# Optimization experiments

Hardware: AMD Instinct MI355X
Metric: run time of the kernel (lower is better)

## Reference

```python
import jax, jax.numpy as jnp
import numpy as np

D_MODEL = 1024
N_HEADS = 16
FEA = 512
BATCH = 16
D_FF = 2048
HALF = D_MODEL // 2  # d_model / 2**fd_num with fd_num=1
INV_SQRT2 = 1.0 / np.sqrt(2.0).astype(np.float32)


def conv1d_circ(x, w, b):
    # x: (B, C_in, L); w: (C_out, C_in, 3); circular padding of 1 each side
    xp = jnp.pad(x, ((0, 0), (0, 0), (1, 1)), mode='wrap')
    y = jax.lax.conv_general_dilated(xp, w, (1,), 'VALID',
                                     dimension_numbers=('NCH', 'OIH', 'NCH'))
    return y + b[None, :, None]


def layer_norm(x, g, b):
    m = jnp.mean(x, axis=-1, keepdims=True)
    v = jnp.mean((x - m) ** 2, axis=-1, keepdims=True)
    return (x - m) / jnp.sqrt(v + 1e-5) * g + b


def setup_inputs() -> dict:
    key = jax.random.key(0)
    ks = jax.random.split(key, 16)
    s = 0.02
    inp = {
        'x': jax.random.normal(ks[0], (BATCH, FEA, D_MODEL), dtype=jnp.float32),
        'Wq': jax.random.normal(ks[1], (D_MODEL, HALF, 3), dtype=jnp.float32) * s,
        'bq': jnp.zeros((D_MODEL,), jnp.float32),
        'Wk': jax.random.normal(ks[2], (D_MODEL, HALF, 3), dtype=jnp.float32) * s,
        'bk': jnp.zeros((D_MODEL,), jnp.float32),
        'Wv': jax.random.normal(ks[3], (D_MODEL, HALF, 3), dtype=jnp.float32) * s,
        'bv': jnp.zeros((D_MODEL,), jnp.float32),
        'uns_w': jax.random.normal(ks[4], (FEA, 2 * FEA, 3), dtype=jnp.float32) * s,
        'uns_b': jnp.zeros((FEA,), jnp.float32),
        'cv_w1': jax.random.normal(ks[5], (D_FF, D_MODEL, 3), dtype=jnp.float32) * s,
        'cv_b1': jnp.zeros((D_FF,), jnp.float32),
        'cv_w2': jax.random.normal(ks[6], (HALF, D_FF, 3), dtype=jnp.float32) * s,
        'cv_b2': jnp.zeros((HALF,), jnp.float32),
        'cv_g': jnp.ones((HALF,), jnp.float32),
        'cv_beta': jnp.zeros((HALF,), jnp.float32),
        'up_w1': jax.random.normal(ks[7], (D_FF, HALF, 3), dtype=jnp.float32) * s,
        'up_b1': jnp.zeros((D_FF,), jnp.float32),
        'up_w2': jax.random.normal(ks[8], (D_MODEL, D_FF, 3), dtype=jnp.float32) * s,
        'up_b2': jnp.zeros((D_MODEL,), jnp.float32),
        'up_g': jnp.ones((D_MODEL,), jnp.float32),
        'up_beta': jnp.zeros((D_MODEL,), jnp.float32),
    }
    return inp


def reference(x, Wq, bq, Wk, bk, Wv, bv, uns_w, uns_b,
              cv_w1, cv_b1, cv_w2, cv_b2, cv_g, cv_beta,
              up_w1, up_b1, up_w2, up_b2, up_g, up_beta):
    x_input = x
    # torch code detaches x before the wavelet transform -> no grad through this branch
    xd = jax.lax.stop_gradient(x)
    # Haar (db1) single-level DWT along last axis (even length -> exact pairwise)
    x1 = (xd[..., 0::2] + xd[..., 1::2]) * INV_SQRT2  # cA: (B, F, HALF)
    x2 = (xd[..., 0::2] - xd[..., 1::2]) * INV_SQRT2  # cD: (B, F, HALF)

    def proj(z, w, b):  # (B, F, HALF) -> (B, F, D_MODEL)
        return conv1d_circ(z.swapaxes(1, 2), w, b).swapaxes(1, 2)

    def heads(z):  # (B, F, D_MODEL) -> (B, H, F, dh)
        b_, f_, _ = z.shape
        return z.reshape(b_, f_, N_HEADS, -1).transpose(0, 2, 1, 3)

    qh, kh, vh = heads(proj(x1, Wq, bq)), heads(proj(x1, Wk, bk)), heads(proj(x1, Wv, bv))
    ql, kl, vl = heads(proj(x2, Wq, bq)), heads(proj(x2, Wk, bk)), heads(proj(x2, Wv, bv))

    scale = 1.0 / np.sqrt(N_HEADS).astype(np.float32)  # note: module scales by sqrt(n_heads)
    b_, f_ = x.shape[0], x.shape[1]

    hp = jax.nn.softmax(jnp.einsum('bhqd,bhkd->bhqk', qh, kl) * scale, axis=-1)
    h_ctx = jnp.einsum('bhqk,bhkd->bhqd', hp, vh).transpose(0, 2, 1, 3).reshape(b_, f_, -1)
    lp = jax.nn.softmax(jnp.einsum('bhqd,bhkd->bhqk', ql, kh) * scale, axis=-1)
    l_ctx = jnp.einsum('bhqk,bhkd->bhqd', lp, vl).transpose(0, 2, 1, 3).reshape(b_, f_, -1)

    ctx = jnp.concatenate([h_ctx, l_ctx], axis=1)          # (B, 2F, D_MODEL)
    ctx = conv1d_circ(ctx, uns_w, uns_b)                    # channels=2F -> F, length=D_MODEL

    # Convlayer: conv over fea axis, channels D_MODEL -> D_FF -> HALF, then LN
    h = conv1d_circ(ctx.swapaxes(1, 2), cv_w1, cv_b1)
    h = conv1d_circ(jax.nn.relu(h), cv_w2, cv_b2)
    ctx = layer_norm(h.swapaxes(1, 2), cv_g, cv_beta)       # (B, F, HALF)

    # upsizeConvlayer: HALF -> D_FF -> D_MODEL, then LN
    h = conv1d_circ(ctx.swapaxes(1, 2), up_w1, up_b1)
    h = conv1d_circ(jax.nn.relu(h), up_w2, up_b2)
    out = layer_norm(h.swapaxes(1, 2), up_g, up_beta)       # (B, F, D_MODEL)
    return out + x_input
```

## Files before the change

kernel.cpp:

```cpp
#include <hip/hip_runtime.h>
#include <hip/hip_bf16.h>

#define B_    16
#define FEA_  512
#define DM_   1024
#define HALF_ 512
#define DFF_  2048

typedef unsigned short u16;
typedef __attribute__((ext_vector_type(8))) short bf16x8;
typedef __attribute__((ext_vector_type(4))) float f32x4;

__device__ __forceinline__ float bf2f(u16 u) {
  union { unsigned int i; float f; } v; v.i = ((unsigned int)u) << 16; return v.f;
}
__device__ __forceinline__ u16 f2bf(float f) {
  union { float f; unsigned int i; } v; v.f = f;
  unsigned int x = v.i;
  return (u16)((x + 0x7fffu + ((x >> 16) & 1u)) >> 16);
}
__device__ __forceinline__ void gload16(const u16* g, u16* l) {
  __builtin_amdgcn_global_load_lds(
      (const __attribute__((address_space(1))) void*)g,
      (__attribute__((address_space(3))) void*)l, 16, 0, 0);
}

__global__ void dwt_kernel(const float* __restrict__ x, u16* __restrict__ x1,
                           u16* __restrict__ x2, int n) {
  int i = blockIdx.x * 256 + threadIdx.x;
  if (i >= n) return;
  float2 v = ((const float2*)x)[i];
  x1[i] = f2bf((v.x + v.y) * 0.70710678118f);
  x2[i] = f2bf((v.x - v.y) * 0.70710678118f);
}

__global__ void wtrans3_kernel(const float* __restrict__ w0, const float* __restrict__ w1,
                               const float* __restrict__ w2, u16* __restrict__ wt,
                               int Cout, int Cin) {
  int n = Cout * Cin * 3;
  int e = blockIdx.x * 256 + threadIdx.x;
  if (e >= 3 * n) return;
  int i = e / n, le = e - i * n;
  const float* w = (i == 0) ? w0 : ((i == 1) ? w1 : w2);
  int co = le / (Cin * 3);
  int r  = le - co * Cin * 3;
  int ci = r / 3;
  int t  = r - ci * 3;
  wt[(size_t)i * n + ((size_t)t * Cout + co) * Cin + ci] = f2bf(w[le]);
}

struct WTSeg { const float* src; u16* dst; int cout, cin, base; };
struct WT5 { WTSeg s[5]; int total; };
__global__ void wtrans5_kernel(WT5 p) {
  int e = blockIdx.x * 256 + threadIdx.x;
  if (e >= p.total) return;
#pragma unroll
  for (int i = 0; i < 5; ++i) {
    int Cin = p.s[i].cin, Cout = p.s[i].cout;
    int n = Cout * Cin * 3;
    int le = e - p.s[i].base;
    if (le >= 0 && le < n) {
      int co = le / (Cin * 3);
      int r  = le - co * Cin * 3;
      int ci = r / 3;
      int t  = r - ci * 3;
      p.s[i].dst[((size_t)t * Cout + co) * Cin + ci] = f2bf(p.s[i].src[le]);
    }
  }
}

#define ZS_GLOAD(c0_)                                                        \
  {                                                                          \
    _Pragma("unroll") for (int i_ = 0; i_ < 5; ++i_) {                       \
      int e_ = tid + i_ * 256;                                               \
      if (e_ < 130 * 8) {                                                    \
        int r_ = e_ >> 3, c_ = e_ & 7;                                       \
        int gl_ = l0 + r_ - 1;                                               \
        if (gl_ < 0) gl_ += L; else if (gl_ >= L) gl_ -= L;                  \
        gload16(Zb + (size_t)gl_ * Cin + (c0_) + ((c_ ^ (r_ & 7)) * 8),      \
                smem + ((size_t)(i_ * 256 + (tid & 192)) * 8));              \
      }                                                                      \
    }                                                                        \
  }
#define WS_ISSUE(t_, c0_, buf_)                                              \
  {                                                                          \
    const u16* Wg_ = Wt + ((size_t)(t_) * Cout + co0) * Cin + (c0_);         \
    int c_ = lane & 7;                                                       \
    _Pragma("unroll") for (int i_ = 0; i_ < 4; ++i_) {                       \
      int rw_ = (i_ * 4 + w) * 8 + (lane >> 3);                              \
      gload16(Wg_ + (size_t)rw_ * Cin + ((c_ ^ (rw_ & 7)) * 8),              \
              &Wb[(buf_)][(i_ * 4 + w) * 8][0]);                             \
    }                                                                        \
  }
#define COMPUTE(t_, buf_)                                                    \
  {                                                                          \
    _Pragma("unroll") for (int ks = 0; ks < 2; ++ks) {                       \
      int s = ks * 4 + g4;                                                   \
      bf16x8 af[4], bfr[4];                                                  \
      _Pragma("unroll") for (int mi = 0; mi < 4; ++mi) {                     \
        int ra = wr * 64 + mi * 16 + row16 + (t_);                           \
        af[mi] = *(const bf16x8*)&Zs[ra][(s ^ (ra & 7)) * 8];                \
      }                                                                      \
      _Pragma("unroll") for (int ni = 0; ni < 4; ++ni) {                     \
        int rb = wc * 64 + ni * 16 + row16;                                  \
        bfr[ni] = *(const bf16x8*)&Wb[(buf_)][rb][(s ^ (rb & 7)) * 8];       \
      }                                                                      \
      __builtin_amdgcn_s_setprio(1);                                         \
      _Pragma("unroll") for (int mi = 0; mi < 4; ++mi)                       \
        _Pragma("unroll") for (int ni = 0; ni < 4; ++ni)                     \
          acc[mi][ni] = __builtin_amdgcn_mfma_f32_16x16x32_bf16(             \
              af[mi], bfr[ni], acc[mi][ni], 0, 0, 0);                        \
      __builtin_amdgcn_s_setprio(0);                                         \
    }                                                                        \
  }
#define COMPUTE2_REG(buf_)                                                   \
  {                                                                          \
    _Pragma("unroll") for (int ks = 0; ks < 2; ++ks) {                       \
      int s = ks * 4 + g4;                                                   \
      bf16x8 bfr[4];                                                         \
      _Pragma("unroll") for (int ni = 0; ni < 4; ++ni) {                     \
        int rb = wc * 64 + ni * 16 + row16;                                  \
        bfr[ni] = *(const bf16x8*)&Wb[(buf_)][rb][(s ^ (rb & 7)) * 8];       \
      }                                                                      \
      __builtin_amdgcn_s_setprio(1);                                         \
      _Pragma("unroll") for (int mi = 0; mi < 4; ++mi)                       \
        _Pragma("unroll") for (int ni = 0; ni < 4; ++ni)                     \
          acc[mi][ni] = __builtin_amdgcn_mfma_f32_16x16x32_bf16(             \
              af2[ks * 4 + mi], bfr[ni], acc[mi][ni], 0, 0, 0);              \
      __builtin_amdgcn_s_setprio(0);                                         \
    }                                                                        \
  }
#define WAIT4 { asm volatile("s_waitcnt vmcnt(4)" ::: "memory");             \
                __builtin_amdgcn_s_barrier(); }

__global__ __launch_bounds__(256, 2) void conv_mfma_kernel(
    const u16* __restrict__ Z, const u16* __restrict__ Wt,
    const float* __restrict__ bias, u16* __restrict__ out,
    int L, int Cin, int Cout, int osl, int osc, int relu) {
  __shared__ __align__(16) u16 smem[130 * 64 + 3 * 128 * 64];
  u16 (*Zs)[64] = (u16(*)[64])smem;
  u16 (*Wb)[128][64] = (u16(*)[128][64])(smem + 130 * 64);
  int l0 = blockIdx.x * 128, co0 = blockIdx.y * 128, b = blockIdx.z;
  int tid = threadIdx.x;
  int lane = tid & 63, w = tid >> 6, wr = w >> 1, wc = w & 1;
  int row16 = lane & 15, g4 = lane >> 4;
  f32x4 acc[4][4];
#pragma unroll
  for (int i = 0; i < 4; ++i)
#pragma unroll
    for (int j = 0; j < 4; ++j) acc[i][j] = (f32x4){0.f, 0.f, 0.f, 0.f};
  const u16* Zb = Z + (size_t)b * L * Cin;

  int ncg = Cin >> 6;
  ZS_GLOAD(0);
  WS_ISSUE(0, 0, 0);
  WS_ISSUE(1, 0, 1);

  for (int cg = 0; cg < ncg; ++cg) {
    int c0 = cg << 6;
    bool lastg = (cg == ncg - 1);
    WAIT4;
    WS_ISSUE(2, c0, 2);
    COMPUTE(0, 0);
    WAIT4;
    if (!lastg) WS_ISSUE(0, c0 + 64, 0);
    COMPUTE(1, 1);
    if (!lastg) {
      WAIT4;
      bf16x8 af2[8];
#pragma unroll
      for (int ks = 0; ks < 2; ++ks) {
        int s = ks * 4 + g4;
#pragma unroll
        for (int mi = 0; mi < 4; ++mi) {
          int ra = wr * 64 + mi * 16 + row16 + 2;
          af2[ks * 4 + mi] = *(const bf16x8*)&Zs[ra][(s ^ (ra & 7)) * 8];
        }
      }
      __builtin_amdgcn_sched_barrier(0);
      asm volatile("s_waitcnt lgkmcnt(0)" ::: "memory");
      __builtin_amdgcn_s_barrier();
      ZS_GLOAD(c0 + 64);
      WS_ISSUE(1, c0 + 64, 1);
      COMPUTE2_REG(2);
    } else {
      asm volatile("s_waitcnt vmcnt(0)" ::: "memory");
      __builtin_amdgcn_s_barrier();
      COMPUTE(2, 2);
    }
  }

  __syncthreads();
  const int TP = 136;
  u16* tile = smem;
  size_t ob = (size_t)b * L * Cout;
  int S, rowbase, colbase;
  if (osc == 1) { S = osl; rowbase = l0; colbase = co0; }
  else          { S = osc; rowbase = co0; colbase = l0; }
#pragma unroll
  for (int ni = 0; ni < 4; ++ni) {
    int c_loc = wc * 64 + ni * 16 + row16;
    float bz = bias[co0 + c_loc];
#pragma unroll
    for (int mi = 0; mi < 4; ++mi) {
#pragma unroll
      for (int r = 0; r < 4; ++r) {
        int l_loc = wr * 64 + mi * 16 + g4 * 4 + r;
        float v = acc[mi][ni][r] + bz;
        if (relu) v = fmaxf(v, 0.f);
        int row = (osc == 1) ? l_loc : c_loc;
        int col = (osc == 1) ? c_loc : l_loc;
        tile[row * TP + col] = f2bf(v);
      }
    }
  }
  __syncthreads();
  for (int e = tid; e < 128 * 16; e += 256) {
    int row = e >> 4, c8 = (e & 15) * 8;
    *(uint4*)(out + ob + (size_t)(rowbase + row) * S + colbase + c8) =
        *(const uint4*)&tile[row * TP + c8];
  }
}

#define AQOFF 0
#define AKOFF 8192
#define AVOFF 20480
#define APOFF 32768
#define AT_Q_STAGE()                                                         \
  { _Pragma("unroll") for (int i_ = 0; i_ < 4; ++i_) {                       \
      int idx_ = tid + i_ * 256; int r_ = idx_ >> 3, c_ = idx_ & 7;          \
      gload16(Qg + (size_t)(q0 + r_) * DM_ + ((c_ ^ (r_ & 7)) * 8),          \
              asm_ + AQOFF + (i_ * 256 + (tid & 192)) * 8); } }
#define AT_K_STAGE(kt_, buf_)                                                \
  { _Pragma("unroll") for (int i_ = 0; i_ < 2; ++i_) {                       \
      int idx_ = tid + i_ * 256; int r_ = idx_ >> 3, c_ = idx_ & 7;          \
      gload16(Kg + (size_t)((kt_) * 64 + r_) * DM_ + ((c_ ^ (r_ & 7)) * 8),  \
              asm_ + AKOFF + (buf_) * 4096 + (i_ * 256 + (tid & 192)) * 8); } }
#define AT_V_STAGE(kt_, buf_)                                                \
  { _Pragma("unroll") for (int i_ = 0; i_ < 2; ++i_) {                       \
      int idx_ = tid + i_ * 256; int r_ = idx_ >> 3, c_ = idx_ & 7;          \
      gload16(Vg + (size_t)r_ * FEA_ + (kt_) * 64 + ((c_ ^ (r_ & 7)) * 8),   \
              asm_ + AVOFF + (buf_) * 4096 + (i_ * 256 + (tid & 192)) * 8); } }
#define LGKM0_BAR { asm volatile("s_waitcnt lgkmcnt(0)" ::: "memory");       \
                    __builtin_amdgcn_s_barrier(); }

__global__ __launch_bounds__(256, 2) void attn_mfma_kernel(
    const u16* __restrict__ qh, const u16* __restrict__ kh, const u16* __restrict__ vhT,
    const u16* __restrict__ ql, const u16* __restrict__ kl, const u16* __restrict__ vlT,
    u16* __restrict__ ctx) {
  __shared__ __align__(16) u16 asm_[36864];
  __shared__ float rsl[2][2][2][32];
  int qt = blockIdx.x, h = blockIdx.y, bz = blockIdx.z;
  int b = bz >> 1, br = bz & 1;
  const u16* Qg = (br ? ql  : qh) + (size_t)b * FEA_ * DM_ + h * 64;
  const u16* Kg = (br ? kh  : kl) + (size_t)b * FEA_ * DM_ + h * 64;
  const u16* Vg = (br ? vlT : vhT) + (size_t)b * DM_ * FEA_ + (size_t)(h * 64) * FEA_;
  int tid = threadIdx.x;
  int lane = tid & 63, w = tid >> 6, wr = w >> 1, wc = w & 1;
  int row16 = lane & 15, g4 = lane >> 4;
  int q0 = qt * 128;

  f32x4 oacc[2][2][2];
  float rsum[2][2][4];
#pragma unroll
  for (int qi = 0; qi < 2; ++qi)
#pragma unroll
    for (int i = 0; i < 2; ++i) {
#pragma unroll
      for (int j = 0; j < 2; ++j) oacc[qi][i][j] = (f32x4){0.f, 0.f, 0.f, 0.f};
#pragma unroll
      for (int r = 0; r < 4; ++r) rsum[qi][i][r] = 0.f;
    }

  AT_Q_STAGE();
  AT_K_STAGE(0, 0); AT_V_STAGE(0, 0);
  AT_K_STAGE(1, 1); AT_V_STAGE(1, 1);

  for (int kt = 0; kt < 8; ++kt) {
    int buf = kt % 3;
    if (kt < 7) asm volatile("s_waitcnt vmcnt(4)" ::: "memory");
    else        asm volatile("s_waitcnt vmcnt(0)" ::: "memory");
    __builtin_amdgcn_s_barrier();
    if (kt < 6) { AT_K_STAGE(kt + 2, (kt + 2) % 3); AT_V_STAGE(kt + 2, (kt + 2) % 3); }
#pragma unroll
    for (int qi = 0; qi < 2; ++qi) {
      f32x4 sacc[2][2];
#pragma unroll
      for (int i = 0; i < 2; ++i)
#pragma unroll
        for (int j = 0; j < 2; ++j) sacc[i][j] = (f32x4){0.f, 0.f, 0.f, 0.f};
#pragma unroll
      for (int ks = 0; ks < 2; ++ks) {
        int s = ks * 4 + g4;
        bf16x8 a0, a1, b0, b1;
        { int ra = qi * 64 + wr * 32 + row16;
          a0 = *(const bf16x8*)&asm_[AQOFF + ra * 64 + ((s ^ (ra & 7)) * 8)]; }
        { int ra = qi * 64 + wr * 32 + 16 + row16;
          a1 = *(const bf16x8*)&asm_[AQOFF + ra * 64 + ((s ^ (ra & 7)) * 8)]; }
        { int rb = wc * 32 + row16;
          b0 = *(const bf16x8*)&asm_[AKOFF + buf * 4096 + rb * 64 + ((s ^ (rb & 7)) * 8)]; }
        { int rb = wc * 32 + 16 + row16;
          b1 = *(const bf16x8*)&asm_[AKOFF + buf * 4096 + rb * 64 + ((s ^ (rb & 7)) * 8)]; }
        __builtin_amdgcn_s_setprio(1);
        sacc[0][0] = __builtin_amdgcn_mfma_f32_16x16x32_bf16(a0, b0, sacc[0][0], 0, 0, 0);
        sacc[0][1] = __builtin_amdgcn_mfma_f32_16x16x32_bf16(a0, b1, sacc[0][1], 0, 0, 0);
        sacc[1][0] = __builtin_amdgcn_mfma_f32_16x16x32_bf16(a1, b0, sacc[1][0], 0, 0, 0);
        sacc[1][1] = __builtin_amdgcn_mfma_f32_16x16x32_bf16(a1, b1, sacc[1][1], 0, 0, 0);
        __builtin_amdgcn_s_setprio(0);
      }
      if (qi == 1) { LGKM0_BAR; }
#pragma unroll
      for (int mi = 0; mi < 2; ++mi)
#pragma unroll
        for (int ni = 0; ni < 2; ++ni)
#pragma unroll
          for (int r = 0; r < 4; ++r) {
            float p = __expf(sacc[mi][ni][r] * 0.25f);
            rsum[qi][mi][r] += p;
            int pr = wr * 32 + mi * 16 + g4 * 4 + r;
            int ck = wc * 32 + ni * 16 + row16;
            asm_[APOFF + pr * 64 + (((ck >> 3) ^ (pr & 7)) * 8 + (ck & 7))] = f2bf(p);
          }
      LGKM0_BAR;
#pragma unroll
      for (int ks = 0; ks < 2; ++ks) {
        int s = ks * 4 + g4;
        bf16x8 a0, a1, b0, b1;
        { int pa = wr * 32 + row16;
          a0 = *(const bf16x8*)&asm_[APOFF + pa * 64 + ((s ^ (pa & 7)) * 8)]; }
        { int pa = wr * 32 + 16 + row16;
          a1 = *(const bf16x8*)&asm_[APOFF + pa * 64 + ((s ^ (pa & 7)) * 8)]; }
        { int rv = wc * 32 + row16;
          b0 = *(const bf16x8*)&asm_[AVOFF + buf * 4096 + rv * 64 + ((s ^ (rv & 7)) * 8)]; }
        { int rv = wc * 32 + 16 + row16;
          b1 = *(const bf16x8*)&asm_[AVOFF + buf * 4096 + rv * 64 + ((s ^ (rv & 7)) * 8)]; }
        __builtin_amdgcn_s_setprio(1);
        oacc[qi][0][0] = __builtin_amdgcn_mfma_f32_16x16x32_bf16(a0, b0, oacc[qi][0][0], 0, 0, 0);
        oacc[qi][0][1] = __builtin_amdgcn_mfma_f32_16x16x32_bf16(a0, b1, oacc[qi][0][1], 0, 0, 0);
        oacc[qi][1][0] = __builtin_amdgcn_mfma_f32_16x16x32_bf16(a1, b0, oacc[qi][1][0], 0, 0, 0);
        oacc[qi][1][1] = __builtin_amdgcn_mfma_f32_16x16x32_bf16(a1, b1, oacc[qi][1][1], 0, 0, 0);
        __builtin_amdgcn_s_setprio(0);
      }
    }
  }

#pragma unroll
  for (int qi = 0; qi < 2; ++qi)
#pragma unroll
    for (int mi = 0; mi < 2; ++mi)
#pragma unroll
      for (int r = 0; r < 4; ++r) {
#pragma unroll
        for (int m = 1; m < 16; m <<= 1)
          rsum[qi][mi][r] += __shfl_xor(rsum[qi][mi][r], m);
      }
  if (row16 == 0) {
#pragma unroll
    for (int qi = 0; qi < 2; ++qi)
#pragma unroll
      for (int mi = 0; mi < 2; ++mi)
#pragma unroll
        for (int r = 0; r < 4; ++r)
          rsl[qi][wr][wc][mi * 16 + g4 * 4 + r] = rsum[qi][mi][r];
  }
  __syncthreads();
#pragma unroll
  for (int qi = 0; qi < 2; ++qi) {
#pragma unroll
    for (int mi = 0; mi < 2; ++mi)
#pragma unroll
      for (int ni = 0; ni < 2; ++ni)
#pragma unroll
        for (int r = 0; r < 4; ++r) {
          int qq = mi * 16 + g4 * 4 + r;
          float denom = rsl[qi][wr][0][qq] + rsl[qi][wr][1][qq];
          float o = oacc[qi][mi][ni][r] / denom;
          int d = wc * 32 + ni * 16 + row16;
          int qc = wr * 32 + qq;
          asm_[APOFF + d * 64 + (((qc >> 3) ^ (d & 7)) * 8 + (qc & 7))] = f2bf(o);
        }
    __syncthreads();
#pragma unroll
    for (int i = 0; i < 2; ++i) {
      int idx = tid + i * 256;
      int r = idx >> 3, c = idx & 7;
      size_t dst = ((size_t)b * DM_ + h * 64 + r) * (2 * FEA_) + br * 512 + q0 + qi * 64 + c * 8;
      *(uint4*)(ctx + dst) = *(const uint4*)&asm_[APOFF + r * 64 + ((c ^ (r & 7)) * 8)];
    }
    if (qi == 0) __syncthreads();
  }
}

template <int RESID>
__global__ void ln_kernel(const u16* __restrict__ in, const float* __restrict__ g,
                          const float* __restrict__ beta, const float* __restrict__ resid,
                          void* __restrict__ outp, int C) {
  int row = blockIdx.x;
  int tid = threadIdx.x;
  const u16* p = in + (size_t)row * C;
  float s = 0.f, ss = 0.f;
  for (int c = tid * 4; c < C; c += 1024) {
    ushort4 u = *(const ushort4*)(p + c);
    float v0 = bf2f(u.x), v1 = bf2f(u.y), v2 = bf2f(u.z), v3 = bf2f(u.w);
    s += v0 + v1 + v2 + v3;
    ss += v0 * v0 + v1 * v1 + v2 * v2 + v3 * v3;
  }
#pragma unroll
  for (int m = 1; m < 64; m <<= 1) { s += __shfl_xor(s, m); ss += __shfl_xor(ss, m); }
  __shared__ float red[2][4];
  int wid = tid >> 6, lane = tid & 63;
  if (lane == 0) { red[0][wid] = s; red[1][wid] = ss; }
  __syncthreads();
  s  = red[0][0] + red[0][1] + red[0][2] + red[0][3];
  ss = red[1][0] + red[1][1] + red[1][2] + red[1][3];
  float m  = s / C;
  float var = ss / C - m * m;
  float inv = rsqrtf(var + 1e-5f);
  for (int c = tid * 4; c < C; c += 1024) {
    ushort4 u = *(const ushort4*)(p + c);
    float4 gg = *(const float4*)(g + c);
    float4 bb = *(const float4*)(beta + c);
    float v0 = (bf2f(u.x) - m) * inv * gg.x + bb.x;
    float v1 = (bf2f(u.y) - m) * inv * gg.y + bb.y;
    float v2 = (bf2f(u.z) - m) * inv * gg.z + bb.z;
    float v3 = (bf2f(u.w) - m) * inv * gg.w + bb.w;
    if (RESID) {
      float4 rr = *(const float4*)(resid + (size_t)row * C + c);
      float4 o = {v0 + rr.x, v1 + rr.y, v2 + rr.z, v3 + rr.w};
      *(float4*)((float*)outp + (size_t)row * C + c) = o;
    } else {
      ushort4 o = {f2bf(v0), f2bf(v1), f2bf(v2), f2bf(v3)};
      *(ushort4*)((u16*)outp + (size_t)row * C + c) = o;
    }
  }
}

extern "C" void kernel_launch(void* const* d_in, const int* in_sizes, int n_in,
                              void* d_out, int out_size, void* d_ws, size_t ws_size,
                              hipStream_t stream) {
  (void)in_sizes; (void)n_in; (void)out_size; (void)ws_size;
  const float* x      = (const float*)d_in[0];
  const float* Wq     = (const float*)d_in[1];
  const float* bq     = (const float*)d_in[2];
  const float* Wk     = (const float*)d_in[3];
  const float* bk     = (const float*)d_in[4];
  const float* Wv     = (const float*)d_in[5];
  const float* bv     = (const float*)d_in[6];
  const float* uns_w  = (const float*)d_in[7];
  const float* uns_b  = (const float*)d_in[8];
  const float* cv_w1  = (const float*)d_in[9];
  const float* cv_b1  = (const float*)d_in[10];
  const float* cv_w2  = (const float*)d_in[11];
  const float* cv_b2  = (const float*)d_in[12];
  const float* cv_g   = (const float*)d_in[13];
  const float* cv_beta= (const float*)d_in[14];
  const float* up_w1  = (const float*)d_in[15];
  const float* up_b1  = (const float*)d_in[16];
  const float* up_w2  = (const float*)d_in[17];
  const float* up_b2  = (const float*)d_in[18];
  const float* up_g   = (const float*)d_in[19];
  const float* up_beta= (const float*)d_in[20];

  char* ws = (char*)d_ws;
  const size_t MB = 1ull << 20;
  u16* x1    = (u16*)(ws + 0);
  u16* x1x2  = x1;
  u16* qhb   = (u16*)(ws + 16 * MB);
  u16* khb   = (u16*)(ws + 48 * MB);
  u16* vhb   = (u16*)(ws + 80 * MB);
  u16* qlb   = (u16*)(ws + 32 * MB);
  u16* klb   = (u16*)(ws + 64 * MB);
  u16* vlb   = (u16*)(ws + 96 * MB);
  u16* wt_proj = (u16*)d_out;
  u16* ctx   = (u16*)d_out;
  u16* wt_uns  = (u16*)(ws + 0);
  u16* wt_cv1  = (u16*)(ws + 4 * MB);
  u16* wt_cv2  = (u16*)(ws + 17 * MB);
  u16* wt_up1  = (u16*)(ws + 24 * MB);
  u16* wt_up2  = (u16*)(ws + 31 * MB);
  u16* ctx2  = (u16*)(ws + 48 * MB);
  u16* h1    = (u16*)(ws + 64 * MB);
  u16* h2    = (u16*)(ws + 96 * MB);
  u16* ctx3  = (u16*)(ws + 104 * MB);
  u16* h3    = (u16*)(ws + 64 * MB);
  u16* h4    = (u16*)(ws + 48 * MB);

  dwt_kernel<<<(B_ * FEA_ * HALF_ + 255) / 256, 256, 0, stream>>>(x, x1, (u16*)(ws + 8 * MB),
                                                                  B_ * FEA_ * HALF_);

  const int NPROJ = DM_ * HALF_ * 3;
  wtrans3_kernel<<<(3 * NPROJ + 255) / 256, 256, 0, stream>>>(Wq, Wk, Wv, wt_proj, DM_, HALF_);

  auto conv = [&](const u16* Z, const u16* wt, const float* bias, u16* out, int L,
                  int Cin, int Cout, int osl, int osc, int relu, int nb) {
    conv_mfma_kernel<<<dim3(L / 128, Cout / 128, nb), 256, 0, stream>>>(
        Z, wt, bias, out, L, Cin, Cout, osl, osc, relu);
  };

  conv(x1x2, wt_proj,              bq, qhb, FEA_, HALF_, DM_, DM_, 1, 0, 32);
  conv(x1x2, wt_proj + NPROJ,      bk, khb, FEA_, HALF_, DM_, DM_, 1, 0, 32);
  conv(x1x2, wt_proj + 2 * NPROJ,  bv, vhb, FEA_, HALF_, DM_, 1, FEA_, 0, 32);

  attn_mfma_kernel<<<dim3(4, 16, 32), 256, 0, stream>>>(qhb, khb, vhb, qlb, klb, vlb, ctx);

  WT5 p;
  int base = 0;
  auto seg = [&](int i, const float* src, u16* dst, int cout, int cin) {
    p.s[i] = {src, dst, cout, cin, base};
    base += cout * cin * 3;
  };
  seg(0, uns_w, wt_uns, FEA_, 2 * FEA_);
  seg(1, cv_w1, wt_cv1, DFF_, DM_);
  seg(2, cv_w2, wt_cv2, HALF_, DFF_);
  seg(3, up_w1, wt_up1, DFF_, HALF_);
  seg(4, up_w2, wt_up2, DM_, DFF_);
  p.total = base;
  wtrans5_kernel<<<(p.total + 255) / 256, 256, 0, stream>>>(p);

  conv(ctx, wt_uns, uns_b, ctx2, DM_, 2 * FEA_, FEA_, 1, DM_, 0, B_);

  conv(ctx2, wt_cv1, cv_b1, h1, FEA_, DM_, DFF_, DFF_, 1, 1, B_);
  conv(h1, wt_cv2, cv_b2, h2, FEA_, DFF_, HALF_, HALF_, 1, 0, B_);
  ln_kernel<0><<<B_ * FEA_, 256, 0, stream>>>(h2, cv_g, cv_beta, nullptr, ctx3, HALF_);

  conv(ctx3, wt_up1, up_b1, h3, FEA_, HALF_, DFF_, DFF_, 1, 1, B_);
  conv(h3, wt_up2, up_b2, h4, FEA_, DFF_, DM_, DM_, 1, 0, B_);
  ln_kernel<1><<<B_ * FEA_, 256, 0, stream>>>(h4, up_g, up_beta, x, d_out, DM_);
}
```

Baseline: 671.4 us.

## Shrink attention query tile to 64 rows and double-buffer K/V for occupancy

The attention kernel now handles 64 query rows per block instead of 128, doubling the grid and halving Q staging, accumulators and shared memory. The K/V pipeline drops from triple buffering with a two-tile lookahead to double buffering with one-tile lookahead, and launch bounds now request three blocks per CU. The aim is more resident blocks and more parallelism per CU. In exchange each K/V tile is loaded twice as often across blocks, and the shallower prefetch with a full vmcnt(0) wait exposes more load latency.

```diff
diff --git a/kernel.cpp b/kernel.cpp
--- a/kernel.cpp
+++ b/kernel.cpp
@@ -223,11 +223,11 @@
 }
 
 #define AQOFF 0
-#define AKOFF 8192
-#define AVOFF 20480
-#define APOFF 32768
+#define AKOFF 4096
+#define AVOFF 12288
+#define APOFF 20480
 #define AT_Q_STAGE()                                                         \
-  { _Pragma("unroll") for (int i_ = 0; i_ < 4; ++i_) {                       \
+  { _Pragma("unroll") for (int i_ = 0; i_ < 2; ++i_) {                       \
       int idx_ = tid + i_ * 256; int r_ = idx_ >> 3, c_ = idx_ & 7;          \
       gload16(Qg + (size_t)(q0 + r_) * DM_ + ((c_ ^ (r_ & 7)) * 8),          \
               asm_ + AQOFF + (i_ * 256 + (tid & 192)) * 8); } }
@@ -244,12 +244,12 @@
 #define LGKM0_BAR { asm volatile("s_waitcnt lgkmcnt(0)" ::: "memory");       \
                     __builtin_amdgcn_s_barrier(); }
 
-__global__ __launch_bounds__(256, 2) void attn_mfma_kernel(
+__global__ __launch_bounds__(256, 3) void attn_mfma_kernel(
     const u16* __restrict__ qh, const u16* __restrict__ kh, const u16* __restrict__ vhT,
     const u16* __restrict__ ql, const u16* __restrict__ kl, const u16* __restrict__ vlT,
     u16* __restrict__ ctx) {
-  __shared__ __align__(16) u16 asm_[36864];
-  __shared__ float rsl[2][2][2][32];
+  __shared__ __align__(16) u16 asm_[24576];
+  __shared__ float rsl[2][2][32];
   int qt = blockIdx.x, h = blockIdx.y, bz = blockIdx.z;
   int b = bz >> 1, br = bz & 1;
   const u16* Qg = (br ? ql  : qh) + (size_t)b * FEA_ * DM_ + h * 64;
@@ -258,136 +258,118 @@
   int tid = threadIdx.x;
   int lane = tid & 63, w = tid >> 6, wr = w >> 1, wc = w & 1;
   int row16 = lane & 15, g4 = lane >> 4;
-  int q0 = qt * 128;
-
-  f32x4 oacc[2][2][2];
-  float rsum[2][2][4];
-#pragma unroll
-  for (int qi = 0; qi < 2; ++qi)
-#pragma unroll
-    for (int i = 0; i < 2; ++i) {
-#pragma unroll
-      for (int j = 0; j < 2; ++j) oacc[qi][i][j] = (f32x4){0.f, 0.f, 0.f, 0.f};
-#pragma unroll
-      for (int r = 0; r < 4; ++r) rsum[qi][i][r] = 0.f;
-    }
+  int q0 = qt * 64;
+
+  f32x4 oacc[2][2];
+  float rsum[2][4];
+#pragma unroll
+  for (int i = 0; i < 2; ++i) {
+#pragma unroll
+    for (int j = 0; j < 2; ++j) oacc[i][j] = (f32x4){0.f, 0.f, 0.f, 0.f};
+#pragma unroll
+    for (int r = 0; r < 4; ++r) rsum[i][r] = 0.f;
+  }
 
   AT_Q_STAGE();
   AT_K_STAGE(0, 0); AT_V_STAGE(0, 0);
-  AT_K_STAGE(1, 1); AT_V_STAGE(1, 1);
 
   for (int kt = 0; kt < 8; ++kt) {
-    int buf = kt % 3;
-    if (kt < 7) asm volatile("s_waitcnt vmcnt(4)" ::: "memory");
-    else        asm volatile("s_waitcnt vmcnt(0)" ::: "memory");
+    int buf = kt & 1;
+    asm volatile("s_waitcnt vmcnt(0)" ::: "memory");
     __builtin_amdgcn_s_barrier();
-    if (kt < 6) { AT_K_STAGE(kt + 2, (kt + 2) % 3); AT_V_STAGE(kt + 2, (kt + 2) % 3); }
-#pragma unroll
-    for (int qi = 0; qi < 2; ++qi) {
-      f32x4 sacc[2][2];
-#pragma unroll
-      for (int i = 0; i < 2; ++i)
-#pragma unroll
-        for (int j = 0; j < 2; ++j) sacc[i][j] = (f32x4){0.f, 0.f, 0.f, 0.f};
-#pragma unroll
-      for (int ks = 0; ks < 2; ++ks) {
-        int s = ks * 4 + g4;
-        bf16x8 a0, a1, b0, b1;
-        { int ra = qi * 64 + wr * 32 + row16;
-          a0 = *(const bf16x8*)&asm_[AQOFF + ra * 64 + ((s ^ (ra & 7)) * 8)]; }
-        { int ra = qi * 64 + wr * 32 + 16 + row16;
-          a1 = *(const bf16x8*)&asm_[AQOFF + ra * 64 + ((s ^ (ra & 7)) * 8)]; }
-        { int rb = wc * 32 + row16;
-          b0 = *(const bf16x8*)&asm_[AKOFF + buf * 4096 + rb * 64 + ((s ^ (rb & 7)) * 8)]; }
-        { int rb = wc * 32 + 16 + row16;
-          b1 = *(const bf16x8*)&asm_[AKOFF + buf * 4096 + rb * 64 + ((s ^ (rb & 7)) * 8)]; }
-        __builtin_amdgcn_s_setprio(1);
-        sacc[0][0] = __builtin_amdgcn_mfma_f32_16x16x32_bf16(a0, b0, sacc[0][0], 0, 0, 0);
-        sacc[0][1] = __builtin_amdgcn_mfma_f32_16x16x32_bf16(a0, b1, sacc[0][1], 0, 0, 0);
-        sacc[1][0] = __builtin_amdgcn_mfma_f32_16x16x32_bf16(a1, b0, sacc[1][0], 0, 0, 0);
-        sacc[1][1] = __builtin_amdgcn_mfma_f32_16x16x32_bf16(a1, b1, sacc[1][1], 0, 0, 0);
-        __builtin_amdgcn_s_setprio(0);
+    if (kt < 7) { AT_K_STAGE(kt + 1, buf ^ 1); AT_V_STAGE(kt + 1, buf ^ 1); }
+    f32x4 sacc[2][2];
+#pragma unroll
+    for (int i = 0; i < 2; ++i)
+#pragma unroll
+      for (int j = 0; j < 2; ++j) sacc[i][j] = (f32x4){0.f, 0.f, 0.f, 0.f};
+#pragma unroll
+    for (int ks = 0; ks < 2; ++ks) {
+      int s = ks * 4 + g4;
+      bf16x8 a0, a1, b0, b1;
+      { int ra = wr * 32 + row16;
+        a0 = *(const bf16x8*)&asm_[AQOFF + ra * 64 + ((s ^ (ra & 7)) * 8)]; }
+      { int ra = wr * 32 + 16 + row16;
+        a1 = *(const bf16x8*)&asm_[AQOFF + ra * 64 + ((s ^ (ra & 7)) * 8)]; }
+      { int rb = wc * 32 + row16;
+        b0 = *(const bf16x8*)&asm_[AKOFF + buf * 4096 + rb * 64 + ((s ^ (rb & 7)) * 8)]; }
+      { int rb = wc * 32 + 16 + row16;
+        b1 = *(const bf16x8*)&asm_[AKOFF + buf * 4096 + rb * 64 + ((s ^ (rb & 7)) * 8)]; }
+      __builtin_amdgcn_s_setprio(1);
+      sacc[0][0] = __builtin_amdgcn_mfma_f32_16x16x32_bf16(a0, b0, sacc[0][0], 0, 0, 0);
+      sacc[0][1] = __builtin_amdgcn_mfma_f32_16x16x32_bf16(a0, b1, sacc[0][1], 0, 0, 0);
+      sacc[1][0] = __builtin_amdgcn_mfma_f32_16x16x32_bf16(a1, b0, sacc[1][0], 0, 0, 0);
+      sacc[1][1] = __builtin_amdgcn_mfma_f32_16x16x32_bf16(a1, b1, sacc[1][1], 0, 0, 0);
+      __builtin_amdgcn_s_setprio(0);
+    }
+#pragma unroll
+    for (int mi = 0; mi < 2; ++mi)
+#pragma unroll
+      for (int ni = 0; ni < 2; ++ni)
+#pragma unroll
+        for (int r = 0; r < 4; ++r) {
+          float p = __expf(sacc[mi][ni][r] * 0.25f);
+          rsum[mi][r] += p;
+          int pr = wr * 32 + mi * 16 + g4 * 4 + r;
+          int ck = wc * 32 + ni * 16 + row16;
+          asm_[APOFF + pr * 64 + (((ck >> 3) ^ (pr & 7)) * 8 + (ck & 7))] = f2bf(p);
+        }
+    LGKM0_BAR;
+#pragma unroll
+    for (int ks = 0; ks < 2; ++ks) {
+      int s = ks * 4 + g4;
+      bf16x8 a0, a1, b0, b1;
+      { int pa = wr * 32 + row16;
+        a0 = *(const bf16x8*)&asm_[APOFF + pa * 64 + ((s ^ (pa & 7)) * 8)]; }
+      { int pa = wr * 32 + 16 + row16;
+        a1 = *(const bf16x8*)&asm_[APOFF + pa * 64 + ((s ^ (pa & 7)) * 8)]; }
+      { int rv = wc * 32 + row16;
+        b0 = *(const bf16x8*)&asm_[AVOFF + buf * 4096 + rv * 64 + ((s ^ (rv & 7)) * 8)]; }
+      { int rv = wc * 32 + 16 + row16;
+        b1 = *(const bf16x8*)&asm_[AVOFF + buf * 4096 + rv * 64 + ((s ^ (rv & 7)) * 8)]; }
+      __builtin_amdgcn_s_setprio(1);
+      oacc[0][0] = __builtin_amdgcn_mfma_f32_16x16x32_bf16(a0, b0, oacc[0][0], 0, 0, 0);
+      oacc[0][1] = __builtin_amdgcn_mfma_f32_16x16x32_bf16(a0, b1, oacc[0][1], 0, 0, 0);
+      oacc[1][0] = __builtin_amdgcn_mfma_f32_16x16x32_bf16(a1, b0, oacc[1][0], 0, 0, 0);
+      oacc[1][1] = __builtin_amdgcn_mfma_f32_16x16x32_bf16(a1, b1, oacc[1][1], 0, 0, 0);
+      __builtin_amdgcn_s_setprio(0);
+    }
+  }
+
+#pragma unroll
+  for (int mi = 0; mi < 2; ++mi)
+#pragma unroll
+    for (int r = 0; r < 4; ++r) {
+#pragma unroll
+      for (int m = 1; m < 16; m <<= 1) rsum[mi][r] += __shfl_xor(rsum[mi][r], m);
+    }
+  if (row16 == 0) {
+#pragma unroll
+    for (int mi = 0; mi < 2; ++mi)
+#pragma unroll
+      for (int r = 0; r < 4; ++r) rsl[wr][wc][mi * 16 + g4 * 4 + r] = rsum[mi][r];
+  }
+  __syncthreads();
+#pragma unroll
+  for (int mi = 0; mi < 2; ++mi)
+#pragma unroll
+    for (int ni = 0; ni < 2; ++ni)
+#pragma unroll
+      for (int r = 0; r < 4; ++r) {
+        int qq = mi * 16 + g4 * 4 + r;
+        float denom = rsl[wr][0][qq] + rsl[wr][1][qq];
+        float o = oacc[mi][ni][r] / denom;
+        int d = wc * 32 + ni * 16 + row16;
+        int qc = wr * 32 + qq;
+        asm_[APOFF + d * 64 + (((qc >> 3) ^ (d & 7)) * 8 + (qc & 7))] = f2bf(o);
       }
-      if (qi == 1) { LGKM0_BAR; }
-#pragma unroll
-      for (int mi = 0; mi < 2; ++mi)
-#pragma unroll
-        for (int ni = 0; ni < 2; ++ni)
-#pragma unroll
-          for (int r = 0; r < 4; ++r) {
-            float p = __expf(sacc[mi][ni][r] * 0.25f);
-            rsum[qi][mi][r] += p;
-            int pr = wr * 32 + mi * 16 + g4 * 4 + r;
-            int ck = wc * 32 + ni * 16 + row16;
-            asm_[APOFF + pr * 64 + (((ck >> 3) ^ (pr & 7)) * 8 + (ck & 7))] = f2bf(p);
-          }
-      LGKM0_BAR;
-#pragma unroll
-      for (int ks = 0; ks < 2; ++ks) {
-        int s = ks * 4 + g4;
-        bf16x8 a0, a1, b0, b1;
-        { int pa = wr * 32 + row16;
-          a0 = *(const bf16x8*)&asm_[APOFF + pa * 64 + ((s ^ (pa & 7)) * 8)]; }
-        { int pa = wr * 32 + 16 + row16;
-          a1 = *(const bf16x8*)&asm_[APOFF + pa * 64 + ((s ^ (pa & 7)) * 8)]; }
-        { int rv = wc * 32 + row16;
-          b0 = *(const bf16x8*)&asm_[AVOFF + buf * 4096 + rv * 64 + ((s ^ (rv & 7)) * 8)]; }
-        { int rv = wc * 32 + 16 + row16;
-          b1 = *(const bf16x8*)&asm_[AVOFF + buf * 4096 + rv * 64 + ((s ^ (rv & 7)) * 8)]; }
-        __builtin_amdgcn_s_setprio(1);
-        oacc[qi][0][0] = __builtin_amdgcn_mfma_f32_16x16x32_bf16(a0, b0, oacc[qi][0][0], 0, 0, 0);
-        oacc[qi][0][1] = __builtin_amdgcn_mfma_f32_16x16x32_bf16(a0, b1, oacc[qi][0][1], 0, 0, 0);
-        oacc[qi][1][0] = __builtin_amdgcn_mfma_f32_16x16x32_bf16(a1, b0, oacc[qi][1][0], 0, 0, 0);
-        oacc[qi][1][1] = __builtin_amdgcn_mfma_f32_16x16x32_bf16(a1, b1, oacc[qi][1][1], 0, 0, 0);
-        __builtin_amdgcn_s_setprio(0);
-      }
-    }
-  }
-
-#pragma unroll
-  for (int qi = 0; qi < 2; ++qi)
-#pragma unroll
-    for (int mi = 0; mi < 2; ++mi)
-#pragma unroll
-      for (int r = 0; r < 4; ++r) {
-#pragma unroll
-        for (int m = 1; m < 16; m <<= 1)
-          rsum[qi][mi][r] += __shfl_xor(rsum[qi][mi][r], m);
-      }
-  if (row16 == 0) {
-#pragma unroll
-    for (int qi = 0; qi < 2; ++qi)
-#pragma unroll
-      for (int mi = 0; mi < 2; ++mi)
-#pragma unroll
-        for (int r = 0; r < 4; ++r)
-          rsl[qi][wr][wc][mi * 16 + g4 * 4 + r] = rsum[qi][mi][r];
-  }
   __syncthreads();
 #pragma unroll
-  for (int qi = 0; qi < 2; ++qi) {
-#pragma unroll
-    for (int mi = 0; mi < 2; ++mi)
-#pragma unroll
-      for (int ni = 0; ni < 2; ++ni)
-#pragma unroll
-        for (int r = 0; r < 4; ++r) {
-          int qq = mi * 16 + g4 * 4 + r;
-          float denom = rsl[qi][wr][0][qq] + rsl[qi][wr][1][qq];
-          float o = oacc[qi][mi][ni][r] / denom;
-          int d = wc * 32 + ni * 16 + row16;
-          int qc = wr * 32 + qq;
-          asm_[APOFF + d * 64 + (((qc >> 3) ^ (d & 7)) * 8 + (qc & 7))] = f2bf(o);
-        }
-    __syncthreads();
-#pragma unroll
-    for (int i = 0; i < 2; ++i) {
-      int idx = tid + i * 256;
-      int r = idx >> 3, c = idx & 7;
-      size_t dst = ((size_t)b * DM_ + h * 64 + r) * (2 * FEA_) + br * 512 + q0 + qi * 64 + c * 8;
-      *(uint4*)(ctx + dst) = *(const uint4*)&asm_[APOFF + r * 64 + ((c ^ (r & 7)) * 8)];
-    }
-    if (qi == 0) __syncthreads();
+  for (int i = 0; i < 2; ++i) {
+    int idx = tid + i * 256;
+    int r = idx >> 3, c = idx & 7;
+    size_t dst = ((size_t)b * DM_ + h * 64 + r) * (2 * FEA_) + br * 512 + q0 + c * 8;
+    *(uint4*)(ctx + dst) = *(const uint4*)&asm_[APOFF + r * 64 + ((c ^ (r & 7)) * 8)];
   }
 }
 
@@ -501,7 +483,7 @@
   conv(x1x2, wt_proj + NPROJ,      bk, khb, FEA_, HALF_, DM_, DM_, 1, 0, 32);
   conv(x1x2, wt_proj + 2 * NPROJ,  bv, vhb, FEA_, HALF_, DM_, 1, FEA_, 0, 32);
 
-  attn_mfma_kernel<<<dim3(4, 16, 32), 256, 0, stream>>>(qhb, khb, vhb, qlb, klb, vlb, ctx);
+  attn_mfma_kernel<<<dim3(8, 16, 32), 256, 0, stream>>>(qhb, khb, vhb, qlb, klb, vlb, ctx);
 
   WT5 p;
   int base = 0;
```

New measurement: 662.6 us. About the same (-1.3%).
